# Kernel optimization log

Measured on AMD Instinct MI355X. Metric: run time of the kernel, lower is better.

## Reference

```python
import jax, jax.numpy as jnp
import numpy as np

N_NODES = 50000
N_EDGES = 1600000
N_GRAPHS = 64
D = 128


def setup_inputs() -> dict:
    key = jax.random.key(0)
    ks = jax.random.split(key, 6)
    x = jax.random.normal(ks[0], (N_NODES, D), dtype=jnp.float32)
    W1 = jax.random.normal(ks[1], (D, D), dtype=jnp.float32) * (1.0 / np.sqrt(D))
    b1 = jnp.zeros((D,), dtype=jnp.float32)
    W2 = jax.random.normal(ks[2], (D, D), dtype=jnp.float32) * (1.0 / np.sqrt(D))
    b2 = jnp.zeros((D,), dtype=jnp.float32)
    edge_index = jax.random.randint(ks[3], (2, N_EDGES), 0, N_NODES, dtype=jnp.int64)
    batch = jnp.sort(jax.random.randint(ks[4], (N_NODES,), 0, N_GRAPHS, dtype=jnp.int64))
    return {"x": x, "W1": W1, "b1": b1, "W2": W2, "b2": b2,
            "edge_index": edge_index, "batch": batch}


def _gcn_conv(x, W, b, src, dst, coef, n_nodes):
    # GCNConv: h = W^T x; out_i = sum_{j->i} norm_ij * h_j + b
    h = x @ W                                  # [N, D_out]
    msg = h[src] * coef[:, None]               # [E+N, D_out] gather + scale
    out = jax.ops.segment_sum(msg, dst, num_segments=n_nodes)
    return out + b


def reference(x, W1, b1, W2, b2, edge_index, batch):
    n_nodes = x.shape[0]
    # add self-loops (PyG GCNConv default add_self_loops=True)
    loop = jnp.arange(n_nodes, dtype=edge_index.dtype)
    src = jnp.concatenate([edge_index[0], loop])
    dst = jnp.concatenate([edge_index[1], loop])
    # symmetric normalization: deg counted on target side incl. self-loops
    deg = jax.ops.segment_sum(jnp.ones_like(dst, dtype=x.dtype), dst,
                              num_segments=n_nodes)
    dinv = jnp.where(deg > 0, jax.lax.rsqrt(deg), 0.0)
    coef = dinv[src] * dinv[dst]               # [E+N]

    h = jax.nn.relu(_gcn_conv(x, W1, b1, src, dst, coef, n_nodes))
    h = jax.nn.relu(_gcn_conv(h, W2, b2, src, dst, coef, n_nodes))

    # global_mean_pool over batch ids
    sums = jax.ops.segment_sum(h, batch, num_segments=N_GRAPHS)
    cnts = jax.ops.segment_sum(jnp.ones((n_nodes,), dtype=h.dtype), batch,
                               num_segments=N_GRAPHS)
    return sums / jnp.maximum(cnts, 1.0)[:, None]
```

## Files before the change

kernel.cpp:

```cpp
#include <hip/hip_runtime.h>
#include <stdint.h>

#define DF 128
#define PAD 80
#define BCAP 8192

typedef __attribute__((ext_vector_type(8))) __bf16 bf16x8;
typedef __attribute__((ext_vector_type(4))) float f32x4;

__device__ inline unsigned bf16rn(float x) {
    unsigned u = __float_as_uint(x);
    return (u + 0x7FFFu + ((u >> 16) & 1u)) >> 16;
}
__device__ inline float4 unpack_bf16x4(uint2 v) {
    float4 r;
    r.x = __uint_as_float(v.x << 16);
    r.y = __uint_as_float(v.x & 0xFFFF0000u);
    r.z = __uint_as_float(v.y << 16);
    r.w = __uint_as_float(v.y & 0xFFFF0000u);
    return r;
}
__device__ inline void addf4(float4& a, float4 f) {
    a.x += f.x; a.y += f.y; a.z += f.z; a.w += f.w;
}

__global__ __launch_bounds__(256) void bucket_kernel(const int* __restrict__ src,
        const int* __restrict__ dst, int* __restrict__ gcursor,
        unsigned* __restrict__ buckets, int E) {
    __shared__ int hist[256];
    __shared__ int base[256];
    __shared__ int loc[256];
    int tid = threadIdx.x;
    hist[tid] = 0; loc[tid] = 0;
    __syncthreads();
    int beg = blockIdx.x * BCAP;
    int end = beg + BCAP; if (end > E) end = E;
    for (int i = beg + tid; i < end; i += 256) {
        int d = dst[i];
        atomicAdd(&hist[d >> 8], 1);
    }
    __syncthreads();
    base[tid] = atomicAdd(&gcursor[tid], hist[tid]);
    __syncthreads();
    for (int i = beg + tid; i < end; i += 256) {
        int d = dst[i];
        int s = __builtin_nontemporal_load(src + i);
        int b = d >> 8;
        int r = atomicAdd(&loc[b], 1);
        int pos = base[b] + r;
        if (pos < BCAP)
            buckets[(size_t)b * BCAP + pos] = ((unsigned)(d & 255) << 16) | (unsigned)s;
    }
}

__global__ __launch_bounds__(256) void csr_kernel(const unsigned* __restrict__ buckets,
        const int* __restrict__ gcursor, unsigned short* __restrict__ csr,
        int* __restrict__ cnt, float* __restrict__ dinv,
        const int* __restrict__ batch, int* __restrict__ gse, int N, int G) {
    __shared__ int nodecnt[256];
    int tid = threadIdx.x;
    nodecnt[tid] = 0;
    __syncthreads();
    int b = blockIdx.x;
    int nb = gcursor[b]; if (nb > BCAP) nb = BCAP;
    const unsigned* __restrict__ bk = buckets + (size_t)b * BCAP;
    for (int i = tid; i < nb; i += 256) {
        unsigned w = bk[i];
        int dl = w >> 16;
        int r = atomicAdd(&nodecnt[dl], 1);
        if (r < PAD)
            csr[(size_t)(b * 256 + dl) * PAD + r] = (unsigned short)(w & 0xFFFFu);
    }
    __syncthreads();
    int node = b * 256 + tid;
    if (node < N) {
        int c = nodecnt[tid];
        cnt[node] = c;
        dinv[node] = rsqrtf((float)(c + 1));
        int bg = batch[node];
        if (node == 0 || batch[node - 1] != bg) gse[bg] = node;
        if (node == N - 1 || batch[node + 1] != bg) gse[G + bg] = node + 1;
    }
}

__global__ __launch_bounds__(256) void gemm_mfma(
    const float* __restrict__ A, const float* __restrict__ W,
    const float* __restrict__ dinv, uint2* __restrict__ g2, int N)
{
    __shared__ unsigned short Wt[128 * 136];
    int tid = threadIdx.x;
    int wv = tid >> 6;
    int l  = tid & 63;
    int lr = l & 15;
    int lk = (l >> 4) * 8;
    int r  = blockIdx.x * 64 + wv * 16 + lr;
    int rc = (r < N) ? r : (N - 1);

    float4 areg[8];
    const float* Arow = A + (size_t)rc * DF;
    #pragma unroll
    for (int ks = 0; ks < 4; ++ks) {
        areg[2 * ks]     = *(const float4*)(Arow + ks * 32 + lk);
        areg[2 * ks + 1] = *(const float4*)(Arow + ks * 32 + lk + 4);
    }

    #pragma unroll
    for (int i = 0; i < 16; ++i) {
        int flat = i * 256 + tid;
        int k = flat >> 5;
        int c4 = (flat & 31) << 2;
        float4 w4 = *(const float4*)(W + (size_t)k * DF + c4);
        Wt[(c4 + 0) * 136 + k] = (unsigned short)bf16rn(w4.x);
        Wt[(c4 + 1) * 136 + k] = (unsigned short)bf16rn(w4.y);
        Wt[(c4 + 2) * 136 + k] = (unsigned short)bf16rn(w4.z);
        Wt[(c4 + 3) * 136 + k] = (unsigned short)bf16rn(w4.w);
    }

    union U8 { unsigned short s[8]; bf16x8 v; };
    bf16x8 aH[4], aL[4];
    #pragma unroll
    for (int ks = 0; ks < 4; ++ks) {
        U8 uh, ul;
        const float* f0 = (const float*)&areg[2 * ks];
        #pragma unroll
        for (int j = 0; j < 8; ++j) {
            float a = f0[j];
            unsigned hb = bf16rn(a);
            float hf = __uint_as_float(hb << 16);
            uh.s[j] = (unsigned short)hb;
            ul.s[j] = (unsigned short)bf16rn(a - hf);
        }
        aH[ks] = uh.v; aL[ks] = ul.v;
    }

    __syncthreads();

    f32x4 zero = {0.f, 0.f, 0.f, 0.f};
    f32x4 acc[8];
    #pragma unroll
    for (int t = 0; t < 8; ++t) acc[t] = zero;

    #pragma unroll
    for (int ks = 0; ks < 4; ++ks) {
        int ko = ks * 32 + lk;
        #pragma unroll
        for (int t = 0; t < 8; ++t) {
            bf16x8 wf = *(const bf16x8*)&Wt[(t * 16 + lr) * 136 + ko];
            acc[t] = __builtin_amdgcn_mfma_f32_16x16x32_bf16(wf, aH[ks], acc[t], 0, 0, 0);
            acc[t] = __builtin_amdgcn_mfma_f32_16x16x32_bf16(wf, aL[ks], acc[t], 0, 0, 0);
        }
    }

    if (r < N) {
        float di = dinv[r];
        int hi4 = l >> 4;
        #pragma unroll
        for (int t = 0; t < 8; ++t) {
            unsigned lo = bf16rn(di * acc[t][0]) | (bf16rn(di * acc[t][1]) << 16);
            unsigned hi = bf16rn(di * acc[t][2]) | (bf16rn(di * acc[t][3]) << 16);
            uint2 o; o.x = lo; o.y = hi;
            g2[(size_t)r * 32 + t * 4 + hi4] = o;
        }
    }
}

template<bool POOL>
__global__ __launch_bounds__(256) void agg_kernel(
    const uint2* __restrict__ g, const unsigned short* __restrict__ csr,
    const int* __restrict__ cnt, const float* __restrict__ dinv,
    const float* __restrict__ bias, float* __restrict__ out,
    const int* __restrict__ batch, float* __restrict__ acc, int n)
{
    __shared__ float hrow[8 * 128];
    __shared__ int gids[8];
    int idx = blockIdx.x * 256 + threadIdx.x;
    int node = idx >> 5;
    int lane = threadIdx.x & 31;
    bool active = node < n;

    float4 a0 = {0,0,0,0}, a1 = {0,0,0,0}, a2 = {0,0,0,0}, a3 = {0,0,0,0};
    float4 o  = {0,0,0,0};

    if (active) {
        int deg = cnt[node]; if (deg > PAD) deg = PAD;
        const unsigned short* __restrict__ row = csr + (size_t)node * PAD;
        a0 = unpack_bf16x4(g[(size_t)node * 32 + lane]);

        int e = 0;
        for (; e + 15 < deg; e += 16) {
            uint4 wA = *(const uint4*)(row + e);
            uint4 wB = *(const uint4*)(row + e + 8);
            uint2 v0 = g[(size_t)(wA.x & 0xFFFFu) * 32 + lane];
            uint2 v1 = g[(size_t)(wA.x >> 16)     * 32 + lane];
            uint2 v2 = g[(size_t)(wA.y & 0xFFFFu) * 32 + lane];
            uint2 v3 = g[(size_t)(wA.y >> 16)     * 32 + lane];
            uint2 v4 = g[(size_t)(wA.z & 0xFFFFu) * 32 + lane];
            uint2 v5 = g[(size_t)(wA.z >> 16)     * 32 + lane];
            uint2 v6 = g[(size_t)(wA.w & 0xFFFFu) * 32 + lane];
            uint2 v7 = g[(size_t)(wA.w >> 16)     * 32 + lane];
            uint2 u0 = g[(size_t)(wB.x & 0xFFFFu) * 32 + lane];
            uint2 u1 = g[(size_t)(wB.x >> 16)     * 32 + lane];
            uint2 u2 = g[(size_t)(wB.y & 0xFFFFu) * 32 + lane];
            uint2 u3 = g[(size_t)(wB.y >> 16)     * 32 + lane];
            uint2 u4 = g[(size_t)(wB.z & 0xFFFFu) * 32 + lane];
            uint2 u5 = g[(size_t)(wB.z >> 16)     * 32 + lane];
            uint2 u6 = g[(size_t)(wB.w & 0xFFFFu) * 32 + lane];
            uint2 u7 = g[(size_t)(wB.w >> 16)     * 32 + lane];
            addf4(a0, unpack_bf16x4(v0)); addf4(a1, unpack_bf16x4(v1));
            addf4(a2, unpack_bf16x4(v2)); addf4(a3, unpack_bf16x4(v3));
            addf4(a0, unpack_bf16x4(v4)); addf4(a1, unpack_bf16x4(v5));
            addf4(a2, unpack_bf16x4(v6)); addf4(a3, unpack_bf16x4(v7));
            addf4(a0, unpack_bf16x4(u0)); addf4(a1, unpack_bf16x4(u1));
            addf4(a2, unpack_bf16x4(u2)); addf4(a3, unpack_bf16x4(u3));
            addf4(a0, unpack_bf16x4(u4)); addf4(a1, unpack_bf16x4(u5));
            addf4(a2, unpack_bf16x4(u6)); addf4(a3, unpack_bf16x4(u7));
        }
        for (; e + 3 < deg; e += 4) {
            int s0 = row[e], s1 = row[e + 1], s2 = row[e + 2], s3 = row[e + 3];
            uint2 v0 = g[(size_t)s0 * 32 + lane];
            uint2 v1 = g[(size_t)s1 * 32 + lane];
            uint2 v2 = g[(size_t)s2 * 32 + lane];
            uint2 v3 = g[(size_t)s3 * 32 + lane];
            addf4(a0, unpack_bf16x4(v0)); addf4(a1, unpack_bf16x4(v1));
            addf4(a2, unpack_bf16x4(v2)); addf4(a3, unpack_bf16x4(v3));
        }
        for (; e < deg; ++e) {
            uint2 v = g[(size_t)row[e] * 32 + lane];
            addf4(a0, unpack_bf16x4(v));
        }
        float sx = (a0.x + a1.x) + (a2.x + a3.x);
        float sy = (a0.y + a1.y) + (a2.y + a3.y);
        float sz = (a0.z + a1.z) + (a2.z + a3.z);
        float sw = (a0.w + a1.w) + (a2.w + a3.w);

        float di = dinv[node];
        float4 b4 = ((const float4*)bias)[lane];
        o.x = fmaxf(fmaf(di, sx, b4.x), 0.f);
        o.y = fmaxf(fmaf(di, sy, b4.y), 0.f);
        o.z = fmaxf(fmaf(di, sz, b4.z), 0.f);
        o.w = fmaxf(fmaf(di, sw, b4.w), 0.f);
        ((float4*)out)[(size_t)node * 32 + lane] = o;
    }

    if (POOL) {
        int lnode = threadIdx.x >> 5;
        float* hr = hrow + lnode * 128 + lane * 4;
        hr[0] = o.x; hr[1] = o.y; hr[2] = o.z; hr[3] = o.w;
        if (lane == 0) gids[lnode] = active ? batch[node] : -1;
        __syncthreads();
        if (threadIdx.x < 128) {
            int c = threadIdx.x;
            int prev = gids[0];
            float s = 0.f;
            #pragma unroll
            for (int rr = 0; rr < 8; ++rr) {
                int gd = gids[rr];
                if (gd < 0) break;
                if (gd != prev) {
                    if (prev >= 0) atomicAdd(&acc[prev * 128 + c], s);
                    s = 0.f; prev = gd;
                }
                s += hrow[rr * 128 + c];
            }
            if (prev >= 0) atomicAdd(&acc[prev * 128 + c], s);
        }
    }
}

__global__ __launch_bounds__(128) void pool_final(
    const float* __restrict__ acc, const int* __restrict__ gse,
    float* __restrict__ out, int G)
{
    int gi = blockIdx.x;
    int c = threadIdx.x;
    int s = gse[gi], e = gse[G + gi];
    out[gi * DF + c] = (e > s) ? (acc[gi * DF + c] / (float)(e - s)) : 0.f;
}

extern "C" void kernel_launch(void* const* d_in, const int* in_sizes, int n_in,
                              void* d_out, int out_size, void* d_ws, size_t ws_size,
                              hipStream_t stream)
{
    const float* x     = (const float*)d_in[0];
    const float* W1    = (const float*)d_in[1];
    const float* b1    = (const float*)d_in[2];
    const float* W2    = (const float*)d_in[3];
    const float* b2    = (const float*)d_in[4];
    const int*   ei    = (const int*)d_in[5];
    const int*   batch = (const int*)d_in[6];

    int N = in_sizes[0] / DF;
    int E = in_sizes[5] / 2;
    int G = out_size / DF;
    const int* src = ei;
    const int* dst = ei + E;

    int nbuck = (N + 255) >> 8;

    char* p = (char*)d_ws;
    int* gcursor = (int*)p; p += (size_t)256 * 4;
    int* gse     = (int*)p; p += (size_t)2 * G * 4;
    float* acc   = (float*)p; p += (size_t)G * DF * 4;
    int* cnt     = (int*)p; p += (size_t)N * 4;
    float* dinv  = (float*)p; p += (size_t)N * 4;
    unsigned* buckets = (unsigned*)p; p += (size_t)nbuck * BCAP * 4;
    unsigned short* csr = (unsigned short*)p; p += (size_t)N * PAD * 2;
    p = (char*)(((uintptr_t)p + 15) & ~(uintptr_t)15);
    uint2* g2 = (uint2*)p; p += (size_t)N * DF * 2;
    float* h  = (float*)p; p += (size_t)N * DF * 4;

    hipMemsetAsync(gcursor, 0, (size_t)(256 + 2 * G + G * DF) * 4, stream);

    const int thr = 256;
    int nb1 = (E + BCAP - 1) / BCAP;

    bucket_kernel<<<nb1, thr, 0, stream>>>(src, dst, gcursor, buckets, E);
    csr_kernel<<<nbuck, thr, 0, stream>>>(buckets, gcursor, csr, cnt, dinv, batch, gse, N, G);

    int gemm_grid = (N + 63) / 64;
    int agg_grid  = (N * 32 + 255) / 256;

    gemm_mfma<<<gemm_grid, thr, 0, stream>>>(x, W1, dinv, g2, N);
    agg_kernel<false><<<agg_grid, thr, 0, stream>>>(g2, csr, cnt, dinv, b1, h, batch, acc, N);
    gemm_mfma<<<gemm_grid, thr, 0, stream>>>(h, W2, dinv, g2, N);
    agg_kernel<true><<<agg_grid, thr, 0, stream>>>(g2, csr, cnt, dinv, b2, h, batch, acc, N);
    pool_final<<<G, 128, 0, stream>>>(acc, gse, (float*)d_out, G);
}
```

Before: 220.1 us.

## Replace global-cursor bucketing with per-chunk cells and split aggregation kernels

The edge bucketing stage now writes each chunk's edges into a private fixed-capacity cell per destination bucket, with a count array, instead of reserving ranges through global atomics on a shared cursor. This removes the histogram pass and the global atomics. The CSR stage then has each thread walk one chunk's cell serially. The aggregation kernel is split into a non-pooling and a pooling variant, and its inner gather unroll drops from 16 to 8 edges. The serial per-cell loop in the CSR stage gives less parallelism, and the smaller unroll reduces memory-level parallelism in the gathers.

```diff
diff --git a/kernel.cpp b/kernel.cpp
--- a/kernel.cpp
+++ b/kernel.cpp
@@ -4,6 +4,7 @@
 #define DF 128
 #define PAD 80
 #define BCAP 8192
+#define CCAP 96
 
 typedef __attribute__((ext_vector_type(8))) __bf16 bf16x8;
 typedef __attribute__((ext_vector_type(4))) float f32x4;
@@ -24,52 +25,54 @@
     a.x += f.x; a.y += f.y; a.z += f.z; a.w += f.w;
 }
 
-__global__ __launch_bounds__(256) void bucket_kernel(const int* __restrict__ src,
-        const int* __restrict__ dst, int* __restrict__ gcursor,
-        unsigned* __restrict__ buckets, int E) {
-    __shared__ int hist[256];
-    __shared__ int base[256];
+__global__ __launch_bounds__(256) void bucket_sp(const int* __restrict__ src,
+        const int* __restrict__ dst, unsigned* __restrict__ buckets,
+        int* __restrict__ cnts, int E, int nchunk, int nbuck) {
     __shared__ int loc[256];
     int tid = threadIdx.x;
-    hist[tid] = 0; loc[tid] = 0;
-    __syncthreads();
-    int beg = blockIdx.x * BCAP;
+    loc[tid] = 0;
+    __syncthreads();
+    int chunk = blockIdx.x;
+    int beg = chunk * BCAP;
     int end = beg + BCAP; if (end > E) end = E;
     for (int i = beg + tid; i < end; i += 256) {
         int d = dst[i];
-        atomicAdd(&hist[d >> 8], 1);
-    }
-    __syncthreads();
-    base[tid] = atomicAdd(&gcursor[tid], hist[tid]);
-    __syncthreads();
-    for (int i = beg + tid; i < end; i += 256) {
-        int d = dst[i];
-        int s = __builtin_nontemporal_load(src + i);
+        int s = src[i];
         int b = d >> 8;
-        int r = atomicAdd(&loc[b], 1);
-        int pos = base[b] + r;
-        if (pos < BCAP)
-            buckets[(size_t)b * BCAP + pos] = ((unsigned)(d & 255) << 16) | (unsigned)s;
-    }
-}
-
-__global__ __launch_bounds__(256) void csr_kernel(const unsigned* __restrict__ buckets,
-        const int* __restrict__ gcursor, unsigned short* __restrict__ csr,
+        int slot = atomicAdd(&loc[b], 1);
+        if (slot < CCAP)
+            buckets[((size_t)b * nchunk + chunk) * CCAP + slot] =
+                ((unsigned)(d & 255) << 16) | (unsigned)s;
+    }
+    __syncthreads();
+    for (int b = tid; b < nbuck; b += 256) {
+        int c = loc[b]; if (c > CCAP) c = CCAP;
+        cnts[(size_t)b * nchunk + chunk] = c;
+    }
+}
+
+__global__ __launch_bounds__(256) void csr_sp(const unsigned* __restrict__ buckets,
+        const int* __restrict__ cnts, unsigned short* __restrict__ csr,
         int* __restrict__ cnt, float* __restrict__ dinv,
-        const int* __restrict__ batch, int* __restrict__ gse, int N, int G) {
+        const int* __restrict__ batch, int* __restrict__ gse,
+        int N, int G, int nchunk) {
     __shared__ int nodecnt[256];
     int tid = threadIdx.x;
     nodecnt[tid] = 0;
     __syncthreads();
     int b = blockIdx.x;
-    int nb = gcursor[b]; if (nb > BCAP) nb = BCAP;
-    const unsigned* __restrict__ bk = buckets + (size_t)b * BCAP;
-    for (int i = tid; i < nb; i += 256) {
-        unsigned w = bk[i];
-        int dl = w >> 16;
-        int r = atomicAdd(&nodecnt[dl], 1);
-        if (r < PAD)
-            csr[(size_t)(b * 256 + dl) * PAD + r] = (unsigned short)(w & 0xFFFFu);
+    const unsigned* __restrict__ bk = buckets + (size_t)b * nchunk * CCAP;
+    const int* __restrict__ cr = cnts + (size_t)b * nchunk;
+    for (int c = tid; c < nchunk; c += 256) {
+        int nb = cr[c];
+        const unsigned* __restrict__ cell = bk + (size_t)c * CCAP;
+        for (int i = 0; i < nb; ++i) {
+            unsigned w = cell[i];
+            int dl = w >> 16;
+            int r = atomicAdd(&nodecnt[dl], 1);
+            if (r < PAD)
+                csr[(size_t)(b * 256 + dl) * PAD + r] = (unsigned short)(w & 0xFFFFu);
+        }
     }
     __syncthreads();
     int node = b * 256 + tid;
@@ -164,8 +167,72 @@
     }
 }
 
-template<bool POOL>
 __global__ __launch_bounds__(256) void agg_kernel(
+    const uint2* __restrict__ g, const unsigned short* __restrict__ csr,
+    const int* __restrict__ cnt, const float* __restrict__ dinv,
+    const float* __restrict__ bias, float* __restrict__ out, int n)
+{
+    int idx = blockIdx.x * 256 + threadIdx.x;
+    int node = idx >> 5;
+    int lane = threadIdx.x & 31;
+    if (node >= n) return;
+    int deg = cnt[node]; if (deg > PAD) deg = PAD;
+    const unsigned short* __restrict__ row = csr + (size_t)node * PAD;
+
+    float4 a0 = unpack_bf16x4(g[(size_t)node * 32 + lane]);
+    float4 a1 = {0.f, 0.f, 0.f, 0.f};
+    float4 a2 = {0.f, 0.f, 0.f, 0.f};
+    float4 a3 = {0.f, 0.f, 0.f, 0.f};
+
+    int e = 0;
+    for (; e + 7 < deg; e += 8) {
+        uint4 w = *(const uint4*)(row + e);
+        int s0 = (int)(w.x & 0xFFFFu), s1 = (int)(w.x >> 16);
+        int s2 = (int)(w.y & 0xFFFFu), s3 = (int)(w.y >> 16);
+        int s4 = (int)(w.z & 0xFFFFu), s5 = (int)(w.z >> 16);
+        int s6 = (int)(w.w & 0xFFFFu), s7 = (int)(w.w >> 16);
+        uint2 v0 = g[(size_t)s0 * 32 + lane];
+        uint2 v1 = g[(size_t)s1 * 32 + lane];
+        uint2 v2 = g[(size_t)s2 * 32 + lane];
+        uint2 v3 = g[(size_t)s3 * 32 + lane];
+        uint2 v4 = g[(size_t)s4 * 32 + lane];
+        uint2 v5 = g[(size_t)s5 * 32 + lane];
+        uint2 v6 = g[(size_t)s6 * 32 + lane];
+        uint2 v7 = g[(size_t)s7 * 32 + lane];
+        addf4(a0, unpack_bf16x4(v0)); addf4(a1, unpack_bf16x4(v1));
+        addf4(a2, unpack_bf16x4(v2)); addf4(a3, unpack_bf16x4(v3));
+        addf4(a0, unpack_bf16x4(v4)); addf4(a1, unpack_bf16x4(v5));
+        addf4(a2, unpack_bf16x4(v6)); addf4(a3, unpack_bf16x4(v7));
+    }
+    for (; e + 3 < deg; e += 4) {
+        int s0 = row[e], s1 = row[e + 1], s2 = row[e + 2], s3 = row[e + 3];
+        uint2 v0 = g[(size_t)s0 * 32 + lane];
+        uint2 v1 = g[(size_t)s1 * 32 + lane];
+        uint2 v2 = g[(size_t)s2 * 32 + lane];
+        uint2 v3 = g[(size_t)s3 * 32 + lane];
+        addf4(a0, unpack_bf16x4(v0)); addf4(a1, unpack_bf16x4(v1));
+        addf4(a2, unpack_bf16x4(v2)); addf4(a3, unpack_bf16x4(v3));
+    }
+    for (; e < deg; ++e) {
+        uint2 v = g[(size_t)row[e] * 32 + lane];
+        addf4(a0, unpack_bf16x4(v));
+    }
+    float sx = (a0.x + a1.x) + (a2.x + a3.x);
+    float sy = (a0.y + a1.y) + (a2.y + a3.y);
+    float sz = (a0.z + a1.z) + (a2.z + a3.z);
+    float sw = (a0.w + a1.w) + (a2.w + a3.w);
+
+    float di = dinv[node];
+    float4 b4 = ((const float4*)bias)[lane];
+    float4 o;
+    o.x = fmaxf(fmaf(di, sx, b4.x), 0.f);
+    o.y = fmaxf(fmaf(di, sy, b4.y), 0.f);
+    o.z = fmaxf(fmaf(di, sz, b4.z), 0.f);
+    o.w = fmaxf(fmaf(di, sw, b4.w), 0.f);
+    ((float4*)out)[(size_t)node * 32 + lane] = o;
+}
+
+__global__ __launch_bounds__(256) void agg_pool(
     const uint2* __restrict__ g, const unsigned short* __restrict__ csr,
     const int* __restrict__ cnt, const float* __restrict__ dinv,
     const float* __restrict__ bias, float* __restrict__ out,
@@ -177,43 +244,35 @@
     int node = idx >> 5;
     int lane = threadIdx.x & 31;
     bool active = node < n;
-
-    float4 a0 = {0,0,0,0}, a1 = {0,0,0,0}, a2 = {0,0,0,0}, a3 = {0,0,0,0};
-    float4 o  = {0,0,0,0};
+    float4 o = {0.f, 0.f, 0.f, 0.f};
 
     if (active) {
         int deg = cnt[node]; if (deg > PAD) deg = PAD;
         const unsigned short* __restrict__ row = csr + (size_t)node * PAD;
-        a0 = unpack_bf16x4(g[(size_t)node * 32 + lane]);
+        float4 a0 = unpack_bf16x4(g[(size_t)node * 32 + lane]);
+        float4 a1 = {0.f, 0.f, 0.f, 0.f};
+        float4 a2 = {0.f, 0.f, 0.f, 0.f};
+        float4 a3 = {0.f, 0.f, 0.f, 0.f};
 
         int e = 0;
-        for (; e + 15 < deg; e += 16) {
-            uint4 wA = *(const uint4*)(row + e);
-            uint4 wB = *(const uint4*)(row + e + 8);
-            uint2 v0 = g[(size_t)(wA.x & 0xFFFFu) * 32 + lane];
-            uint2 v1 = g[(size_t)(wA.x >> 16)     * 32 + lane];
-            uint2 v2 = g[(size_t)(wA.y & 0xFFFFu) * 32 + lane];
-            uint2 v3 = g[(size_t)(wA.y >> 16)     * 32 + lane];
-            uint2 v4 = g[(size_t)(wA.z & 0xFFFFu) * 32 + lane];
-            uint2 v5 = g[(size_t)(wA.z >> 16)     * 32 + lane];
-            uint2 v6 = g[(size_t)(wA.w & 0xFFFFu) * 32 + lane];
-            uint2 v7 = g[(size_t)(wA.w >> 16)     * 32 + lane];
-            uint2 u0 = g[(size_t)(wB.x & 0xFFFFu) * 32 + lane];
-            uint2 u1 = g[(size_t)(wB.x >> 16)     * 32 + lane];
-            uint2 u2 = g[(size_t)(wB.y & 0xFFFFu) * 32 + lane];
-            uint2 u3 = g[(size_t)(wB.y >> 16)     * 32 + lane];
-            uint2 u4 = g[(size_t)(wB.z & 0xFFFFu) * 32 + lane];
-            uint2 u5 = g[(size_t)(wB.z >> 16)     * 32 + lane];
-            uint2 u6 = g[(size_t)(wB.w & 0xFFFFu) * 32 + lane];
-            uint2 u7 = g[(size_t)(wB.w >> 16)     * 32 + lane];
+        for (; e + 7 < deg; e += 8) {
+            uint4 w = *(const uint4*)(row + e);
+            int s0 = (int)(w.x & 0xFFFFu), s1 = (int)(w.x >> 16);
+            int s2 = (int)(w.y & 0xFFFFu), s3 = (int)(w.y >> 16);
+            int s4 = (int)(w.z & 0xFFFFu), s5 = (int)(w.z >> 16);
+            int s6 = (int)(w.w & 0xFFFFu), s7 = (int)(w.w >> 16);
+            uint2 v0 = g[(size_t)s0 * 32 + lane];
+            uint2 v1 = g[(size_t)s1 * 32 + lane];
+            uint2 v2 = g[(size_t)s2 * 32 + lane];
+            uint2 v3 = g[(size_t)s3 * 32 + lane];
+            uint2 v4 = g[(size_t)s4 * 32 + lane];
+            uint2 v5 = g[(size_t)s5 * 32 + lane];
+            uint2 v6 = g[(size_t)s6 * 32 + lane];
+            uint2 v7 = g[(size_t)s7 * 32 + lane];
             addf4(a0, unpack_bf16x4(v0)); addf4(a1, unpack_bf16x4(v1));
             addf4(a2, unpack_bf16x4(v2)); addf4(a3, unpack_bf16x4(v3));
             addf4(a0, unpack_bf16x4(v4)); addf4(a1, unpack_bf16x4(v5));
             addf4(a2, unpack_bf16x4(v6)); addf4(a3, unpack_bf16x4(v7));
-            addf4(a0, unpack_bf16x4(u0)); addf4(a1, unpack_bf16x4(u1));
-            addf4(a2, unpack_bf16x4(u2)); addf4(a3, unpack_bf16x4(u3));
-            addf4(a0, unpack_bf16x4(u4)); addf4(a1, unpack_bf16x4(u5));
-            addf4(a2, unpack_bf16x4(u6)); addf4(a3, unpack_bf16x4(u7));
         }
         for (; e + 3 < deg; e += 4) {
             int s0 = row[e], s1 = row[e + 1], s2 = row[e + 2], s3 = row[e + 3];
@@ -242,28 +301,26 @@
         ((float4*)out)[(size_t)node * 32 + lane] = o;
     }
 
-    if (POOL) {
-        int lnode = threadIdx.x >> 5;
-        float* hr = hrow + lnode * 128 + lane * 4;
-        hr[0] = o.x; hr[1] = o.y; hr[2] = o.z; hr[3] = o.w;
-        if (lane == 0) gids[lnode] = active ? batch[node] : -1;
-        __syncthreads();
-        if (threadIdx.x < 128) {
-            int c = threadIdx.x;
-            int prev = gids[0];
-            float s = 0.f;
-            #pragma unroll
-            for (int rr = 0; rr < 8; ++rr) {
-                int gd = gids[rr];
-                if (gd < 0) break;
-                if (gd != prev) {
-                    if (prev >= 0) atomicAdd(&acc[prev * 128 + c], s);
-                    s = 0.f; prev = gd;
-                }
-                s += hrow[rr * 128 + c];
+    int lnode = threadIdx.x >> 5;
+    float* hr = hrow + lnode * 128 + lane * 4;
+    hr[0] = o.x; hr[1] = o.y; hr[2] = o.z; hr[3] = o.w;
+    if (lane == 0) gids[lnode] = active ? batch[node] : -1;
+    __syncthreads();
+    if (threadIdx.x < 128) {
+        int c = threadIdx.x;
+        int prev = gids[0];
+        float s = 0.f;
+        #pragma unroll
+        for (int rr = 0; rr < 8; ++rr) {
+            int gd = gids[rr];
+            if (gd < 0) break;
+            if (gd != prev) {
+                if (prev >= 0) atomicAdd(&acc[prev * 128 + c], s);
+                s = 0.f; prev = gd;
             }
-            if (prev >= 0) atomicAdd(&acc[prev * 128 + c], s);
-        }
+            s += hrow[rr * 128 + c];
+        }
+        if (prev >= 0) atomicAdd(&acc[prev * 128 + c], s);
     }
 }
 
@@ -295,34 +352,34 @@
     const int* src = ei;
     const int* dst = ei + E;
 
-    int nbuck = (N + 255) >> 8;
+    int nbuck  = (N + 255) >> 8;
+    int nchunk = (E + BCAP - 1) / BCAP;
 
     char* p = (char*)d_ws;
-    int* gcursor = (int*)p; p += (size_t)256 * 4;
     int* gse     = (int*)p; p += (size_t)2 * G * 4;
     float* acc   = (float*)p; p += (size_t)G * DF * 4;
     int* cnt     = (int*)p; p += (size_t)N * 4;
     float* dinv  = (float*)p; p += (size_t)N * 4;
-    unsigned* buckets = (unsigned*)p; p += (size_t)nbuck * BCAP * 4;
+    int* cnts    = (int*)p; p += (size_t)nbuck * nchunk * 4;
+    unsigned* buckets = (unsigned*)p; p += (size_t)nbuck * nchunk * CCAP * 4;
     unsigned short* csr = (unsigned short*)p; p += (size_t)N * PAD * 2;
     p = (char*)(((uintptr_t)p + 15) & ~(uintptr_t)15);
     uint2* g2 = (uint2*)p; p += (size_t)N * DF * 2;
     float* h  = (float*)p; p += (size_t)N * DF * 4;
 
-    hipMemsetAsync(gcursor, 0, (size_t)(256 + 2 * G + G * DF) * 4, stream);
+    hipMemsetAsync(gse, 0, (size_t)(2 * G + G * DF) * 4, stream);
 
     const int thr = 256;
-    int nb1 = (E + BCAP - 1) / BCAP;
-
-    bucket_kernel<<<nb1, thr, 0, stream>>>(src, dst, gcursor, buckets, E);
-    csr_kernel<<<nbuck, thr, 0, stream>>>(buckets, gcursor, csr, cnt, dinv, batch, gse, N, G);
+
+    bucket_sp<<<nchunk, thr, 0, stream>>>(src, dst, buckets, cnts, E, nchunk, nbuck);
+    csr_sp<<<nbuck, thr, 0, stream>>>(buckets, cnts, csr, cnt, dinv, batch, gse, N, G, nchunk);
 
     int gemm_grid = (N + 63) / 64;
     int agg_grid  = (N * 32 + 255) / 256;
 
     gemm_mfma<<<gemm_grid, thr, 0, stream>>>(x, W1, dinv, g2, N);
-    agg_kernel<false><<<agg_grid, thr, 0, stream>>>(g2, csr, cnt, dinv, b1, h, batch, acc, N);
+    agg_kernel<<<agg_grid, thr, 0, stream>>>(g2, csr, cnt, dinv, b1, h, N);
     gemm_mfma<<<gemm_grid, thr, 0, stream>>>(h, W2, dinv, g2, N);
-    agg_kernel<true><<<agg_grid, thr, 0, stream>>>(g2, csr, cnt, dinv, b2, h, batch, acc, N);
+    agg_pool<<<agg_grid, thr, 0, stream>>>(g2, csr, cnt, dinv, b2, h, batch, acc, N);
     pool_final<<<G, 128, 0, stream>>>(acc, gse, (float*)d_out, G);
 }
```

Result: slower. 231.7 us (+5.3%).
